# Optimization experiments

Measured on AMD Instinct MI355X. Metric: run time of the kernel, lower is better.

Reference implementation:

```python
import jax, jax.numpy as jnp
import numpy as np

N = 50000      # num nodes
E = 800000     # num edges (avg degree 16)
F_IN = 64      # num_node_features
H = 128        # hidden_channels (GatedGraphConv out_channels)
C = 16         # num_classes
L = 3          # num_layers


def setup_inputs() -> dict:
    key = jax.random.key(0)
    ks = jax.random.split(key, 9)
    s = 0.05
    x = jax.random.normal(ks[0], (N, F_IN), dtype=jnp.float32)
    edge_index = jax.random.randint(ks[1], (2, E), 0, N, dtype=jnp.int64)
    # GatedGraphConv per-layer message weights [L, H, H]
    W = jax.random.normal(ks[2], (L, H, H), dtype=jnp.float32) * s
    # GRUCell params (torch layout: rows ordered [r, z, n])
    w_ih = jax.random.normal(ks[3], (3 * H, H), dtype=jnp.float32) * s
    w_hh = jax.random.normal(ks[4], (3 * H, H), dtype=jnp.float32) * s
    b_ih = jax.random.normal(ks[5], (3 * H,), dtype=jnp.float32) * s
    b_hh = jax.random.normal(ks[6], (3 * H,), dtype=jnp.float32) * s
    # final classifier
    lin_w = jax.random.normal(ks[7], (C, H), dtype=jnp.float32) * s
    lin_b = jax.random.normal(ks[8], (C,), dtype=jnp.float32) * s
    return {"x": x, "edge_index": edge_index, "W": W, "w_ih": w_ih,
            "w_hh": w_hh, "b_ih": b_ih, "b_hh": b_hh,
            "lin_w": lin_w, "lin_b": lin_b}


def _gru_cell(m, h, w_ih, w_hh, b_ih, b_hh):
    # torch.nn.GRUCell: gates ordered r, z, n
    gi = m @ w_ih.T + b_ih   # [N, 3H]
    gh = h @ w_hh.T + b_hh   # [N, 3H]
    ir, iz, in_ = jnp.split(gi, 3, axis=1)
    hr, hz, hn = jnp.split(gh, 3, axis=1)
    r = jax.nn.sigmoid(ir + hr)
    z = jax.nn.sigmoid(iz + hz)
    n = jnp.tanh(in_ + r * hn)
    return (1.0 - z) * n + z * h


def reference(x, edge_index, W, w_ih, w_hh, b_ih, b_hh, lin_w, lin_b):
    # GatedGraphConv: zero-pad x to out_channels
    h = jnp.pad(x, ((0, 0), (0, H - F_IN)))  # [N, H]
    src = edge_index[0]  # message source (x_j)
    dst = edge_index[1]  # aggregation target
    for i in range(L):  # small fixed layer count
        m = h @ W[i]                                      # [N, H]
        agg = jax.ops.segment_sum(m[src], dst, num_segments=N)  # scatter-add
        h = _gru_cell(agg, h, w_ih, w_hh, b_ih, b_hh)
    out = h @ lin_w.T + lin_b                             # [N, C]
    return jax.nn.log_softmax(out, axis=1)
```

## Files before the change

### kernel.cpp

```cpp
#include <hip/hip_runtime.h>
#include <hip/hip_bf16.h>
#include <math.h>

#define H 128

typedef __bf16 bf16x8 __attribute__((ext_vector_type(8)));
typedef float f32x4 __attribute__((ext_vector_type(4)));
typedef __hip_bfloat16 bf16;

__device__ __forceinline__ bf16x8 ldb8(const bf16* p) {
  return *(const bf16x8*)(const void*)p;
}
__device__ __forceinline__ bf16x8 ldb8o(const bf16* base, unsigned byteoff) {
  return *(const bf16x8*)(const void*)((const char*)base + byteoff);
}
__device__ __forceinline__ float fsig(float x) {
  return __fdividef(1.f, 1.f + __expf(-x));
}
__device__ __forceinline__ float ftanh(float x) {
  float x2 = fminf(fmaxf(2.f * x, -80.f), 80.f);
  float t = __expf(x2);
  return __fdividef(t - 1.f, t + 1.f);
}

__global__ __launch_bounds__(256) void k_prep(const float* __restrict__ x,
                                              bf16* __restrict__ hb,
                                              const float* __restrict__ whh,
                                              bf16* __restrict__ whhb,
                                              const float* __restrict__ W,
                                              const float* __restrict__ wih,
                                              bf16* __restrict__ G,
                                              const int* __restrict__ dst,
                                              int* __restrict__ deg,
                                              int N, int E) {
  int i = blockIdx.x * 256 + threadIdx.x;
  int NH_ = N * H;
  if (i < NH_) {
    int f = i & (H - 1);
    int n = i >> 7;
    hb[i] = __float2bfloat16((f < 64) ? x[n * 64 + f] : 0.f);
    return;
  }
  i -= NH_;
  if (i < 3 * H * H) {
    whhb[i] = __float2bfloat16(whh[i]);
    return;
  }
  i -= 3 * H * H;
  if (i < 3 * 3 * H * H) {
    int l = i / (3 * H * H);
    int r = i % (3 * H * H);
    int j = r >> 7;
    int k = r & (H - 1);
    const float4* a = (const float4*)(wih + (size_t)j * H);
    const float4* b = (const float4*)(W + (size_t)l * H * H + (size_t)k * H);
    float s = 0.f;
#pragma unroll
    for (int q = 0; q < 32; q++) {
      float4 av = a[q], bv = b[q];
      s += av.x * bv.x + av.y * bv.y + av.z * bv.z + av.w * bv.w;
    }
    G[i] = __float2bfloat16(s);
    return;
  }
  i -= 3 * 3 * H * H;
  if (i < E) atomicAdd(&deg[dst[i]], 1);
}

__global__ __launch_bounds__(256) void k_bsum(const int* __restrict__ deg,
                                              int* __restrict__ bsums, int N) {
  __shared__ int ws[4];
  int t = threadIdx.x;
  int i = blockIdx.x * 256 + t;
  int v = (i < N) ? deg[i] : 0;
#pragma unroll
  for (int d = 1; d < 64; d <<= 1) v += __shfl_xor(v, d, 64);
  if ((t & 63) == 0) ws[t >> 6] = v;
  __syncthreads();
  if (t == 0) bsums[blockIdx.x] = ws[0] + ws[1] + ws[2] + ws[3];
}

__global__ __launch_bounds__(256) void k_bscan(int* __restrict__ bsums, int nb) {
  __shared__ int ws[4];
  int t = threadIdx.x;
  int lane = t & 63, w = t >> 6;
  int v = (t < nb) ? bsums[t] : 0;
  int s = v;
#pragma unroll
  for (int d = 1; d < 64; d <<= 1) {
    int u = __shfl_up(s, d, 64);
    if (lane >= d) s += u;
  }
  if (lane == 63) ws[w] = s;
  __syncthreads();
  int woff = 0;
  if (w >= 1) woff += ws[0];
  if (w >= 2) woff += ws[1];
  if (w >= 3) woff += ws[2];
  if (t < nb) bsums[t] = woff + s - v;
}

__global__ __launch_bounds__(256) void k_scan2(const int* __restrict__ deg,
                                               const int* __restrict__ bsums,
                                               int* __restrict__ rowptr,
                                               int* __restrict__ cursor,
                                               int N, int E) {
  __shared__ int ws[4];
  int t = threadIdx.x;
  int lane = t & 63, w = t >> 6;
  int i = blockIdx.x * 256 + t;
  int v = (i < N) ? deg[i] : 0;
  int s = v;
#pragma unroll
  for (int d = 1; d < 64; d <<= 1) {
    int u = __shfl_up(s, d, 64);
    if (lane >= d) s += u;
  }
  if (lane == 63) ws[w] = s;
  __syncthreads();
  int woff = 0;
  if (w >= 1) woff += ws[0];
  if (w >= 2) woff += ws[1];
  if (w >= 3) woff += ws[2];
  int excl = bsums[blockIdx.x] + woff + s - v;
  if (i < N) { rowptr[i] = excl; cursor[i] = excl; }
  if (i == 0) rowptr[N] = E;
}

__global__ __launch_bounds__(256) void k_fill(const int* __restrict__ src,
                                              const int* __restrict__ dst,
                                              int* __restrict__ cursor,
                                              int* __restrict__ csr_src, int E) {
  int e = blockIdx.x * 256 + threadIdx.x;
  if (e < E) {
    int pos = atomicAdd(&cursor[dst[e]], 1);
    csr_src[pos] = src[e];
  }
}

#define ASTRIDE 136
#define FSTRIDE 132
__global__ __launch_bounds__(512) void k_layer(const bf16* __restrict__ hbin,
                                               bf16* __restrict__ hbout,
                                               const bf16* __restrict__ Gl,
                                               const bf16* __restrict__ whhb,
                                               const float* __restrict__ bih,
                                               const float* __restrict__ bhh,
                                               const int* __restrict__ rowptr,
                                               const int* __restrict__ csr_src,
                                               const float* __restrict__ lw,
                                               const float* __restrict__ lb,
                                               float* __restrict__ out,
                                               int N) {
  __shared__ bf16 SH[64 * ASTRIDE];
  bf16* As = SH;
  bf16* Hs = SH + 32 * ASTRIDE;
  int t = threadIdx.x;
  int lane = t & 63;
  int wu = __builtin_amdgcn_readfirstlane(t >> 6);
  int row0 = blockIdx.x * 32;

  {
    int rl = t >> 4;
    int cc = t & 15;
    int row = row0 + rl; if (row > N - 1) row = N - 1;
    *(bf16x8*)(&Hs[rl * ASTRIDE + cc * 8]) = ldb8(hbin + (size_t)row * H + cc * 8);
  }

  int base = row0 + wu * 4;
  int rp[5];
#pragma unroll
  for (int j = 0; j < 5; j++) {
    int rw = base + j; if (rw > N) rw = N;
    rp[j] = rowptr[rw];
  }

  int e4 = lane >> 4;
  int c = lane & 15;
  unsigned coff = (unsigned)c << 4;

  int idxr[4];
#pragma unroll
  for (int rr = 0; rr < 4; rr++) {
    int rb = rp[rr];
    int n = rp[rr + 1] - rb; if (n > 64) n = 64;
    idxr[rr] = (lane < n) ? csr_src[rb + lane] : 0;
  }

  float acc[4][8];
#pragma unroll
  for (int rr = 0; rr < 4; rr++)
#pragma unroll
    for (int j = 0; j < 8; j++) acc[rr][j] = 0.f;

#pragma unroll
  for (int rr = 0; rr < 4; rr++) {
    int n = rp[rr + 1] - rp[rr];
    bf16x8 vv[8];
    float sc[8];
#pragma unroll
    for (int k = 0; k < 8; k++) {
      int s = e4 + 4 * k;
      int on = s < n;
      int ie = __shfl(idxr[rr], on ? s : 0, 64);
      vv[k] = ldb8o(hbin, ((unsigned)ie << 8) | coff);
      sc[k] = on ? 1.f : 0.f;
    }
#pragma unroll
    for (int k = 0; k < 8; k++) {
#pragma unroll
      for (int j = 0; j < 8; j++)
        acc[rr][j] = fmaf(sc[k], (float)vv[k][j], acc[rr][j]);
    }
    if (n > 32) {
      int hi = (n < 64) ? n : 64;
      for (int s0 = 32; s0 < hi; s0 += 4) {
        int s = s0 + e4;
        int on = s < hi;
        int ie = __shfl(idxr[rr], on ? s : 0, 64);
        bf16x8 v = ldb8o(hbin, ((unsigned)ie << 8) | coff);
        float scl = on ? 1.f : 0.f;
#pragma unroll
        for (int j = 0; j < 8; j++) acc[rr][j] = fmaf(scl, (float)v[j], acc[rr][j]);
      }
      int rb = rp[rr], re = rp[rr + 1];
      for (int b0 = rb + 64; b0 < re; b0 += 64) {
        int n2 = re - b0; if (n2 > 64) n2 = 64;
        int idx2 = (lane < n2) ? csr_src[b0 + lane] : 0;
        for (int s0 = 0; s0 < n2; s0 += 4) {
          int s = s0 + e4;
          int on = s < n2;
          int ie = __shfl(idx2, on ? s : 0, 64);
          bf16x8 v = ldb8o(hbin, ((unsigned)ie << 8) | coff);
          float scl = on ? 1.f : 0.f;
#pragma unroll
          for (int j = 0; j < 8; j++) acc[rr][j] = fmaf(scl, (float)v[j], acc[rr][j]);
        }
      }
    }
  }

#pragma unroll
  for (int rr = 0; rr < 4; rr++) {
#pragma unroll
    for (int j = 0; j < 8; j++) {
      acc[rr][j] += __shfl_xor(acc[rr][j], 16, 64);
      acc[rr][j] += __shfl_xor(acc[rr][j], 32, 64);
    }
    if (e4 == 0) {
      int rl = wu * 4 + rr;
      bf16x8 o;
#pragma unroll
      for (int j = 0; j < 8; j++) o[j] = (__bf16)acc[rr][j];
      *(bf16x8*)(&As[rl * ASTRIDE + c * 8]) = o;
    }
  }
  __syncthreads();

  int r = lane & 15, quad = lane >> 4, laneK = quad * 8;
  unsigned col = (unsigned)(wu * 16 + r);
  unsigned wg0 = col << 8;
  unsigned wg1 = (1u << 15) | wg0;
  unsigned wg2 = (2u << 15) | wg0;

  f32x4 aIR[2], aIZ[2], aIN[2], aHR[2], aHZ[2], aHN[2];
#pragma unroll
  for (int q = 0; q < 2; q++) {
    aIR[q] = (f32x4){0.f, 0.f, 0.f, 0.f};
    aIZ[q] = aIR[q]; aIN[q] = aIR[q];
    aHR[q] = aIR[q]; aHZ[q] = aIR[q]; aHN[q] = aIR[q];
  }

#pragma unroll
  for (int kb = 0; kb < 4; kb++) {
    int ko = kb * 32 + laneK;
    unsigned ko2 = (unsigned)(ko << 1);
    bf16x8 a0 = *(const bf16x8*)(&As[r * ASTRIDE + ko]);
    bf16x8 a1 = *(const bf16x8*)(&As[(16 + r) * ASTRIDE + ko]);
    bf16x8 h0 = *(const bf16x8*)(&Hs[r * ASTRIDE + ko]);
    bf16x8 h1 = *(const bf16x8*)(&Hs[(16 + r) * ASTRIDE + ko]);
    bf16x8 gr = ldb8o(Gl, wg0 | ko2);
    aIR[0] = __builtin_amdgcn_mfma_f32_16x16x32_bf16(a0, gr, aIR[0], 0, 0, 0);
    aIR[1] = __builtin_amdgcn_mfma_f32_16x16x32_bf16(a1, gr, aIR[1], 0, 0, 0);
    bf16x8 gz = ldb8o(Gl, wg1 | ko2);
    aIZ[0] = __builtin_amdgcn_mfma_f32_16x16x32_bf16(a0, gz, aIZ[0], 0, 0, 0);
    aIZ[1] = __builtin_amdgcn_mfma_f32_16x16x32_bf16(a1, gz, aIZ[1], 0, 0, 0);
    bf16x8 gn = ldb8o(Gl, wg2 | ko2);
    aIN[0] = __builtin_amdgcn_mfma_f32_16x16x32_bf16(a0, gn, aIN[0], 0, 0, 0);
    aIN[1] = __builtin_amdgcn_mfma_f32_16x16x32_bf16(a1, gn, aIN[1], 0, 0, 0);
    bf16x8 ur = ldb8o(whhb, wg0 | ko2);
    aHR[0] = __builtin_amdgcn_mfma_f32_16x16x32_bf16(h0, ur, aHR[0], 0, 0, 0);
    aHR[1] = __builtin_amdgcn_mfma_f32_16x16x32_bf16(h1, ur, aHR[1], 0, 0, 0);
    bf16x8 uz = ldb8o(whhb, wg1 | ko2);
    aHZ[0] = __builtin_amdgcn_mfma_f32_16x16x32_bf16(h0, uz, aHZ[0], 0, 0, 0);
    aHZ[1] = __builtin_amdgcn_mfma_f32_16x16x32_bf16(h1, uz, aHZ[1], 0, 0, 0);
    bf16x8 un = ldb8o(whhb, wg2 | ko2);
    aHN[0] = __builtin_amdgcn_mfma_f32_16x16x32_bf16(h0, un, aHN[0], 0, 0, 0);
    aHN[1] = __builtin_amdgcn_mfma_f32_16x16x32_bf16(h1, un, aHN[1], 0, 0, 0);
  }

  float bir = bih[col], biz = bih[H + col], bin = bih[2 * H + col];
  float bhr = bhh[col], bhz = bhh[H + col], bhn = bhh[2 * H + col];
  float hpv[2][4];
#pragma unroll
  for (int q = 0; q < 2; q++) {
#pragma unroll
    for (int i = 0; i < 4; i++) {
      int lrow = q * 16 + quad * 4 + i;
      float rg = fsig(aIR[q][i] + bir + aHR[q][i] + bhr);
      float zg = fsig(aIZ[q][i] + biz + aHZ[q][i] + bhz);
      float ng = ftanh(aIN[q][i] + bin + rg * (aHN[q][i] + bhn));
      float hold = __bfloat162float(Hs[lrow * ASTRIDE + col]);
      hpv[q][i] = (1.f - zg) * ng + zg * hold;
    }
  }
  __syncthreads();

  bf16* Sb = SH;
  float* Sf = (float*)SH;
#pragma unroll
  for (int q = 0; q < 2; q++) {
#pragma unroll
    for (int i = 0; i < 4; i++) {
      int lrow = q * 16 + quad * 4 + i;
      if (out) Sf[lrow * FSTRIDE + col] = hpv[q][i];
      else Sb[lrow * ASTRIDE + col] = __float2bfloat16(hpv[q][i]);
    }
  }
  __syncthreads();

  if (!out) {
    int rl = t >> 4;
    int cc = t & 15;
    int row = row0 + rl;
    if (row < N) {
      bf16x8 v = *(const bf16x8*)(&Sb[rl * ASTRIDE + cc * 8]);
      *(bf16x8*)(hbout + (size_t)row * H + cc * 8) = v;
    }
  } else {
    int cc = lane & 15;
    int q2 = lane >> 4;
    f32x4 wv[8];
    const float* wrow = lw + (size_t)cc * H + q2 * 32;
#pragma unroll
    for (int k = 0; k < 8; k++) wv[k] = *(const f32x4*)(wrow + k * 4);
    float bias = lb[cc];
#pragma unroll
    for (int rr = 0; rr < 4; rr++) {
      int lrow = wu * 4 + rr;
      int row = row0 + lrow;
      if (row >= N) continue;
      const float* hrow = &Sf[lrow * FSTRIDE + q2 * 32];
      float p = 0.f;
#pragma unroll
      for (int k = 0; k < 8; k++) {
        f32x4 hv = *(const f32x4*)(hrow + k * 4);
        p += hv[0] * wv[k][0] + hv[1] * wv[k][1] + hv[2] * wv[k][2] + hv[3] * wv[k][3];
      }
      p += __shfl_xor(p, 16, 64);
      p += __shfl_xor(p, 32, 64);
      float z = p + bias;
      float mx = z;
#pragma unroll
      for (int d = 1; d < 16; d <<= 1) mx = fmaxf(mx, __shfl_xor(mx, d, 64));
      float e = expf(z - mx);
      float ssum = e;
#pragma unroll
      for (int d = 1; d < 16; d <<= 1) ssum += __shfl_xor(ssum, d, 64);
      if (q2 == 0) out[(size_t)row * 16 + cc] = z - mx - logf(ssum);
    }
  }
}

extern "C" void kernel_launch(void* const* d_in, const int* in_sizes, int n_in,
                              void* d_out, int out_size, void* d_ws, size_t ws_size,
                              hipStream_t stream) {
  const float* x   = (const float*)d_in[0];
  const int*   ei  = (const int*)d_in[1];
  const float* W   = (const float*)d_in[2];
  const float* wih = (const float*)d_in[3];
  const float* whh = (const float*)d_in[4];
  const float* bih = (const float*)d_in[5];
  const float* bhh = (const float*)d_in[6];
  const float* lw  = (const float*)d_in[7];
  const float* lb  = (const float*)d_in[8];
  float* out = (float*)d_out;

  int N = in_sizes[0] / 64;
  int E = in_sizes[1] / 2;
  const int* src = ei;
  const int* dst = ei + E;

  size_t NH = (size_t)N * H;
  bf16* hb0  = (bf16*)d_ws;
  bf16* hb1  = hb0 + NH;
  bf16* Gb   = hb1 + NH;
  bf16* whhb = Gb + 3 * 3 * H * H;
  int* deg     = (int*)(whhb + 3 * H * H);
  int* rowptr  = deg + N;
  int* cursor  = rowptr + N + 1;
  int* bsums   = cursor + N;
  int* csr_src = bsums + 256;

  int nb_e = (E + 255) / 256;
  int nb_n = (N + 255) / 256;

  hipMemsetAsync(deg, 0, (size_t)N * sizeof(int), stream);
  int totalPrep = (int)NH + 3 * H * H + 3 * 3 * H * H + E;
  k_prep<<<(totalPrep + 255) / 256, 256, 0, stream>>>(x, hb0, whh, whhb, W, wih,
                                                      Gb, dst, deg, N, E);
  k_bsum<<<nb_n, 256, 0, stream>>>(deg, bsums, N);
  k_bscan<<<1, 256, 0, stream>>>(bsums, nb_n);
  k_scan2<<<nb_n, 256, 0, stream>>>(deg, bsums, rowptr, cursor, N, E);
  k_fill<<<nb_e, 256, 0, stream>>>(src, dst, cursor, csr_src, E);

  int nb_layer = (N + 31) / 32;
  bf16* hbp[2] = {hb0, hb1};
  for (int l = 0; l < 3; l++) {
    bf16* hin  = hbp[l & 1];
    bf16* hout = hbp[(l + 1) & 1];
    k_layer<<<nb_layer, 512, 0, stream>>>(hin, hout, Gb + (size_t)l * 3 * H * H,
                                          whhb, bih, bhh, rowptr, csr_src,
                                          lw, lb, (l == 2) ? out : nullptr, N);
  }
}
```

Before: 410.9 us.

## Halve rows per block to 16 and add short-degree gather fast path

The layer kernel now runs 256-thread blocks over 16 destination rows instead of 512-thread blocks over 32. Each wave computes 32 GRU output columns for a single 16-row MFMA tile, where before it computed 16 columns for two row tiles. This raises the occupancy hint and doubles the number of blocks, at the cost of loading each weight fragment once per 16 rows instead of once per 32. The neighbour gather gets a fast path for rows with at most 16 edges, issuing 4 slot loads instead of 8, which cuts wasted masked loads at the average degree of 16.

Measured after the change: 467.6 us. 13.8% more time.

```diff
diff --git a/kernel.cpp b/kernel.cpp
--- a/kernel.cpp
+++ b/kernel.cpp
@@ -21,6 +21,28 @@
   float x2 = fminf(fmaxf(2.f * x, -80.f), 80.f);
   float t = __expf(x2);
   return __fdividef(t - 1.f, t + 1.f);
+}
+
+template <int KB, int KE>
+__device__ __forceinline__ void gslots(const bf16* __restrict__ hbin, int idxw,
+                                       int n, int e4, unsigned coff,
+                                       float* __restrict__ acc) {
+  bf16x8 vv[KE - KB];
+  float sc[KE - KB];
+#pragma unroll
+  for (int k = KB; k < KE; k++) {
+    int s = e4 + 4 * k;
+    int on = s < n;
+    int ie = __shfl(idxw, on ? s : 0, 64);
+    vv[k - KB] = ldb8o(hbin, ((unsigned)ie << 8) | coff);
+    sc[k - KB] = on ? 1.f : 0.f;
+  }
+#pragma unroll
+  for (int k = 0; k < KE - KB; k++) {
+#pragma unroll
+    for (int j = 0; j < 8; j++)
+      acc[j] = fmaf(sc[k], (float)vv[k][j], acc[j]);
+  }
 }
 
 __global__ __launch_bounds__(256) void k_prep(const float* __restrict__ x,
@@ -140,7 +162,7 @@
 
 #define ASTRIDE 136
 #define FSTRIDE 132
-__global__ __launch_bounds__(512) void k_layer(const bf16* __restrict__ hbin,
+__global__ __launch_bounds__(256, 4) void k_layer(const bf16* __restrict__ hbin,
                                                bf16* __restrict__ hbout,
                                                const bf16* __restrict__ Gl,
                                                const bf16* __restrict__ whhb,
@@ -152,13 +174,13 @@
                                                const float* __restrict__ lb,
                                                float* __restrict__ out,
                                                int N) {
-  __shared__ bf16 SH[64 * ASTRIDE];
+  __shared__ bf16 SH[32 * ASTRIDE];
   bf16* As = SH;
-  bf16* Hs = SH + 32 * ASTRIDE;
+  bf16* Hs = SH + 16 * ASTRIDE;
   int t = threadIdx.x;
   int lane = t & 63;
   int wu = __builtin_amdgcn_readfirstlane(t >> 6);
-  int row0 = blockIdx.x * 32;
+  int row0 = blockIdx.x * 16;
 
   {
     int rl = t >> 4;
@@ -196,45 +218,34 @@
 #pragma unroll
   for (int rr = 0; rr < 4; rr++) {
     int n = rp[rr + 1] - rp[rr];
-    bf16x8 vv[8];
-    float sc[8];
-#pragma unroll
-    for (int k = 0; k < 8; k++) {
-      int s = e4 + 4 * k;
-      int on = s < n;
-      int ie = __shfl(idxr[rr], on ? s : 0, 64);
-      vv[k] = ldb8o(hbin, ((unsigned)ie << 8) | coff);
-      sc[k] = on ? 1.f : 0.f;
-    }
-#pragma unroll
-    for (int k = 0; k < 8; k++) {
-#pragma unroll
-      for (int j = 0; j < 8; j++)
-        acc[rr][j] = fmaf(sc[k], (float)vv[k][j], acc[rr][j]);
-    }
-    if (n > 32) {
-      int hi = (n < 64) ? n : 64;
-      for (int s0 = 32; s0 < hi; s0 += 4) {
-        int s = s0 + e4;
-        int on = s < hi;
-        int ie = __shfl(idxr[rr], on ? s : 0, 64);
-        bf16x8 v = ldb8o(hbin, ((unsigned)ie << 8) | coff);
-        float scl = on ? 1.f : 0.f;
-#pragma unroll
-        for (int j = 0; j < 8; j++) acc[rr][j] = fmaf(scl, (float)v[j], acc[rr][j]);
-      }
-      int rb = rp[rr], re = rp[rr + 1];
-      for (int b0 = rb + 64; b0 < re; b0 += 64) {
-        int n2 = re - b0; if (n2 > 64) n2 = 64;
-        int idx2 = (lane < n2) ? csr_src[b0 + lane] : 0;
-        for (int s0 = 0; s0 < n2; s0 += 4) {
+    if (n <= 16) {
+      gslots<0, 4>(hbin, idxr[rr], n, e4, coff, acc[rr]);
+    } else {
+      gslots<0, 8>(hbin, idxr[rr], n, e4, coff, acc[rr]);
+      if (n > 32) {
+        int hi = (n < 64) ? n : 64;
+        for (int s0 = 32; s0 < hi; s0 += 4) {
           int s = s0 + e4;
-          int on = s < n2;
-          int ie = __shfl(idx2, on ? s : 0, 64);
+          int on = s < hi;
+          int ie = __shfl(idxr[rr], on ? s : 0, 64);
           bf16x8 v = ldb8o(hbin, ((unsigned)ie << 8) | coff);
           float scl = on ? 1.f : 0.f;
 #pragma unroll
           for (int j = 0; j < 8; j++) acc[rr][j] = fmaf(scl, (float)v[j], acc[rr][j]);
+        }
+        int rb = rp[rr], re = rp[rr + 1];
+        for (int b0 = rb + 64; b0 < re; b0 += 64) {
+          int n2 = re - b0; if (n2 > 64) n2 = 64;
+          int idx2 = (lane < n2) ? csr_src[b0 + lane] : 0;
+          for (int s0 = 0; s0 < n2; s0 += 4) {
+            int s = s0 + e4;
+            int on = s < n2;
+            int ie = __shfl(idx2, on ? s : 0, 64);
+            bf16x8 v = ldb8o(hbin, ((unsigned)ie << 8) | coff);
+            float scl = on ? 1.f : 0.f;
+#pragma unroll
+            for (int j = 0; j < 8; j++) acc[rr][j] = fmaf(scl, (float)v[j], acc[rr][j]);
+          }
         }
       }
     }
@@ -258,17 +269,15 @@
   __syncthreads();
 
   int r = lane & 15, quad = lane >> 4, laneK = quad * 8;
-  unsigned col = (unsigned)(wu * 16 + r);
-  unsigned wg0 = col << 8;
-  unsigned wg1 = (1u << 15) | wg0;
-  unsigned wg2 = (2u << 15) | wg0;
+  unsigned col0 = (unsigned)(wu * 32 + r);
+  unsigned wgA[2] = {col0 << 8, (col0 + 16) << 8};
 
   f32x4 aIR[2], aIZ[2], aIN[2], aHR[2], aHZ[2], aHN[2];
 #pragma unroll
-  for (int q = 0; q < 2; q++) {
-    aIR[q] = (f32x4){0.f, 0.f, 0.f, 0.f};
-    aIZ[q] = aIR[q]; aIN[q] = aIR[q];
-    aHR[q] = aIR[q]; aHZ[q] = aIR[q]; aHN[q] = aIR[q];
+  for (int g = 0; g < 2; g++) {
+    aIR[g] = (f32x4){0.f, 0.f, 0.f, 0.f};
+    aIZ[g] = aIR[g]; aIN[g] = aIR[g];
+    aHR[g] = aIR[g]; aHZ[g] = aIR[g]; aHN[g] = aIR[g];
   }
 
 #pragma unroll
@@ -276,42 +285,39 @@
     int ko = kb * 32 + laneK;
     unsigned ko2 = (unsigned)(ko << 1);
     bf16x8 a0 = *(const bf16x8*)(&As[r * ASTRIDE + ko]);
-    bf16x8 a1 = *(const bf16x8*)(&As[(16 + r) * ASTRIDE + ko]);
     bf16x8 h0 = *(const bf16x8*)(&Hs[r * ASTRIDE + ko]);
-    bf16x8 h1 = *(const bf16x8*)(&Hs[(16 + r) * ASTRIDE + ko]);
-    bf16x8 gr = ldb8o(Gl, wg0 | ko2);
-    aIR[0] = __builtin_amdgcn_mfma_f32_16x16x32_bf16(a0, gr, aIR[0], 0, 0, 0);
-    aIR[1] = __builtin_amdgcn_mfma_f32_16x16x32_bf16(a1, gr, aIR[1], 0, 0, 0);
-    bf16x8 gz = ldb8o(Gl, wg1 | ko2);
-    aIZ[0] = __builtin_amdgcn_mfma_f32_16x16x32_bf16(a0, gz, aIZ[0], 0, 0, 0);
-    aIZ[1] = __builtin_amdgcn_mfma_f32_16x16x32_bf16(a1, gz, aIZ[1], 0, 0, 0);
-    bf16x8 gn = ldb8o(Gl, wg2 | ko2);
-    aIN[0] = __builtin_amdgcn_mfma_f32_16x16x32_bf16(a0, gn, aIN[0], 0, 0, 0);
-    aIN[1] = __builtin_amdgcn_mfma_f32_16x16x32_bf16(a1, gn, aIN[1], 0, 0, 0);
-    bf16x8 ur = ldb8o(whhb, wg0 | ko2);
-    aHR[0] = __builtin_amdgcn_mfma_f32_16x16x32_bf16(h0, ur, aHR[0], 0, 0, 0);
-    aHR[1] = __builtin_amdgcn_mfma_f32_16x16x32_bf16(h1, ur, aHR[1], 0, 0, 0);
-    bf16x8 uz = ldb8o(whhb, wg1 | ko2);
-    aHZ[0] = __builtin_amdgcn_mfma_f32_16x16x32_bf16(h0, uz, aHZ[0], 0, 0, 0);
-    aHZ[1] = __builtin_amdgcn_mfma_f32_16x16x32_bf16(h1, uz, aHZ[1], 0, 0, 0);
-    bf16x8 un = ldb8o(whhb, wg2 | ko2);
-    aHN[0] = __builtin_amdgcn_mfma_f32_16x16x32_bf16(h0, un, aHN[0], 0, 0, 0);
-    aHN[1] = __builtin_amdgcn_mfma_f32_16x16x32_bf16(h1, un, aHN[1], 0, 0, 0);
-  }
-
-  float bir = bih[col], biz = bih[H + col], bin = bih[2 * H + col];
-  float bhr = bhh[col], bhz = bhh[H + col], bhn = bhh[2 * H + col];
+#pragma unroll
+    for (int g = 0; g < 2; g++) {
+      unsigned w0 = wgA[g] | ko2;
+      bf16x8 gr = ldb8o(Gl, w0);
+      aIR[g] = __builtin_amdgcn_mfma_f32_16x16x32_bf16(a0, gr, aIR[g], 0, 0, 0);
+      bf16x8 gz = ldb8o(Gl, (1u << 15) | w0);
+      aIZ[g] = __builtin_amdgcn_mfma_f32_16x16x32_bf16(a0, gz, aIZ[g], 0, 0, 0);
+      bf16x8 gn = ldb8o(Gl, (2u << 15) | w0);
+      aIN[g] = __builtin_amdgcn_mfma_f32_16x16x32_bf16(a0, gn, aIN[g], 0, 0, 0);
+      bf16x8 ur = ldb8o(whhb, w0);
+      aHR[g] = __builtin_amdgcn_mfma_f32_16x16x32_bf16(h0, ur, aHR[g], 0, 0, 0);
+      bf16x8 uz = ldb8o(whhb, (1u << 15) | w0);
+      aHZ[g] = __builtin_amdgcn_mfma_f32_16x16x32_bf16(h0, uz, aHZ[g], 0, 0, 0);
+      bf16x8 un = ldb8o(whhb, (2u << 15) | w0);
+      aHN[g] = __builtin_amdgcn_mfma_f32_16x16x32_bf16(h0, un, aHN[g], 0, 0, 0);
+    }
+  }
+
   float hpv[2][4];
 #pragma unroll
-  for (int q = 0; q < 2; q++) {
+  for (int g = 0; g < 2; g++) {
+    int col = wu * 32 + g * 16 + r;
+    float bir = bih[col], biz = bih[H + col], bin = bih[2 * H + col];
+    float bhr = bhh[col], bhz = bhh[H + col], bhn = bhh[2 * H + col];
 #pragma unroll
     for (int i = 0; i < 4; i++) {
-      int lrow = q * 16 + quad * 4 + i;
-      float rg = fsig(aIR[q][i] + bir + aHR[q][i] + bhr);
-      float zg = fsig(aIZ[q][i] + biz + aHZ[q][i] + bhz);
-      float ng = ftanh(aIN[q][i] + bin + rg * (aHN[q][i] + bhn));
+      int lrow = quad * 4 + i;
+      float rg = fsig(aIR[g][i] + bir + aHR[g][i] + bhr);
+      float zg = fsig(aIZ[g][i] + biz + aHZ[g][i] + bhz);
+      float ng = ftanh(aIN[g][i] + bin + rg * (aHN[g][i] + bhn));
       float hold = __bfloat162float(Hs[lrow * ASTRIDE + col]);
-      hpv[q][i] = (1.f - zg) * ng + zg * hold;
+      hpv[g][i] = (1.f - zg) * ng + zg * hold;
     }
   }
   __syncthreads();
@@ -319,12 +325,13 @@
   bf16* Sb = SH;
   float* Sf = (float*)SH;
 #pragma unroll
-  for (int q = 0; q < 2; q++) {
+  for (int g = 0; g < 2; g++) {
+    int col = wu * 32 + g * 16 + r;
 #pragma unroll
     for (int i = 0; i < 4; i++) {
-      int lrow = q * 16 + quad * 4 + i;
-      if (out) Sf[lrow * FSTRIDE + col] = hpv[q][i];
-      else Sb[lrow * ASTRIDE + col] = __float2bfloat16(hpv[q][i]);
+      int lrow = quad * 4 + i;
+      if (out) Sf[lrow * FSTRIDE + col] = hpv[g][i];
+      else Sb[lrow * ASTRIDE + col] = __float2bfloat16(hpv[g][i]);
     }
   }
   __syncthreads();
@@ -414,12 +421,12 @@
   k_scan2<<<nb_n, 256, 0, stream>>>(deg, bsums, rowptr, cursor, N, E);
   k_fill<<<nb_e, 256, 0, stream>>>(src, dst, cursor, csr_src, E);
 
-  int nb_layer = (N + 31) / 32;
+  int nb_layer = (N + 15) / 16;
   bf16* hbp[2] = {hb0, hb1};
   for (int l = 0; l < 3; l++) {
     bf16* hin  = hbp[l & 1];
     bf16* hout = hbp[(l + 1) & 1];
-    k_layer<<<nb_layer, 512, 0, stream>>>(hin, hout, Gb + (size_t)l * 3 * H * H,
+    k_layer<<<nb_layer, 256, 0, stream>>>(hin, hout, Gb + (size_t)l * 3 * H * H,
                                           whhb, bih, bhh, rowptr, csr_src,
                                           lw, lb, (l == 2) ? out : nullptr, N);
   }
```

## Halve rows per layer block and fold block-sum into degree atomics

Applied to the files above, without the earlier changes.

The layer kernel now processes 16 rows per 512-thread block instead of 32. Each wave gathers 2 rows instead of 4, and the GRU MFMA step runs one 16-row tile. This doubles the block count, which is meant to give more parallelism and lower register pressure for the latency-bound neighbour gather. The cost is that the G and W_hh weight fragments are reloaded for every 16 rows instead of every 32. Separately, the k_bsum kernel is removed: per-256-node block sums are now accumulated with a second atomicAdd in the prep kernel, saving a launch but adding atomic contention on about 196 counters.

Result: slower. 928.2 us (+125.9%).

```diff
diff --git a/kernel.cpp b/kernel.cpp
--- a/kernel.cpp
+++ b/kernel.cpp
@@ -32,6 +32,7 @@
                                               bf16* __restrict__ G,
                                               const int* __restrict__ dst,
                                               int* __restrict__ deg,
+                                              int* __restrict__ bsums,
                                               int N, int E) {
   int i = blockIdx.x * 256 + threadIdx.x;
   int NH_ = N * H;
@@ -64,20 +65,11 @@
     return;
   }
   i -= 3 * 3 * H * H;
-  if (i < E) atomicAdd(&deg[dst[i]], 1);
-}
-
-__global__ __launch_bounds__(256) void k_bsum(const int* __restrict__ deg,
-                                              int* __restrict__ bsums, int N) {
-  __shared__ int ws[4];
-  int t = threadIdx.x;
-  int i = blockIdx.x * 256 + t;
-  int v = (i < N) ? deg[i] : 0;
-#pragma unroll
-  for (int d = 1; d < 64; d <<= 1) v += __shfl_xor(v, d, 64);
-  if ((t & 63) == 0) ws[t >> 6] = v;
-  __syncthreads();
-  if (t == 0) bsums[blockIdx.x] = ws[0] + ws[1] + ws[2] + ws[3];
+  if (i < E) {
+    int d = dst[i];
+    atomicAdd(&deg[d], 1);
+    atomicAdd(&bsums[d >> 8], 1);
+  }
 }
 
 __global__ __launch_bounds__(256) void k_bscan(int* __restrict__ bsums, int nb) {
@@ -152,25 +144,25 @@
                                                const float* __restrict__ lb,
                                                float* __restrict__ out,
                                                int N) {
-  __shared__ bf16 SH[64 * ASTRIDE];
+  __shared__ bf16 SH[32 * ASTRIDE];
   bf16* As = SH;
-  bf16* Hs = SH + 32 * ASTRIDE;
+  bf16* Hs = SH + 16 * ASTRIDE;
   int t = threadIdx.x;
   int lane = t & 63;
   int wu = __builtin_amdgcn_readfirstlane(t >> 6);
-  int row0 = blockIdx.x * 32;
-
-  {
+  int row0 = blockIdx.x * 16;
+
+  if (t < 256) {
     int rl = t >> 4;
     int cc = t & 15;
     int row = row0 + rl; if (row > N - 1) row = N - 1;
     *(bf16x8*)(&Hs[rl * ASTRIDE + cc * 8]) = ldb8(hbin + (size_t)row * H + cc * 8);
   }
 
-  int base = row0 + wu * 4;
-  int rp[5];
-#pragma unroll
-  for (int j = 0; j < 5; j++) {
+  int base = row0 + wu * 2;
+  int rp[3];
+#pragma unroll
+  for (int j = 0; j < 3; j++) {
     int rw = base + j; if (rw > N) rw = N;
     rp[j] = rowptr[rw];
   }
@@ -179,22 +171,22 @@
   int c = lane & 15;
   unsigned coff = (unsigned)c << 4;
 
-  int idxr[4];
-#pragma unroll
-  for (int rr = 0; rr < 4; rr++) {
+  int idxr[2];
+#pragma unroll
+  for (int rr = 0; rr < 2; rr++) {
     int rb = rp[rr];
     int n = rp[rr + 1] - rb; if (n > 64) n = 64;
     idxr[rr] = (lane < n) ? csr_src[rb + lane] : 0;
   }
 
-  float acc[4][8];
-#pragma unroll
-  for (int rr = 0; rr < 4; rr++)
+  float acc[2][8];
+#pragma unroll
+  for (int rr = 0; rr < 2; rr++)
 #pragma unroll
     for (int j = 0; j < 8; j++) acc[rr][j] = 0.f;
 
 #pragma unroll
-  for (int rr = 0; rr < 4; rr++) {
+  for (int rr = 0; rr < 2; rr++) {
     int n = rp[rr + 1] - rp[rr];
     bf16x8 vv[8];
     float sc[8];
@@ -241,14 +233,14 @@
   }
 
 #pragma unroll
-  for (int rr = 0; rr < 4; rr++) {
+  for (int rr = 0; rr < 2; rr++) {
 #pragma unroll
     for (int j = 0; j < 8; j++) {
       acc[rr][j] += __shfl_xor(acc[rr][j], 16, 64);
       acc[rr][j] += __shfl_xor(acc[rr][j], 32, 64);
     }
     if (e4 == 0) {
-      int rl = wu * 4 + rr;
+      int rl = wu * 2 + rr;
       bf16x8 o;
 #pragma unroll
       for (int j = 0; j < 8; j++) o[j] = (__bf16)acc[rr][j];
@@ -263,79 +255,62 @@
   unsigned wg1 = (1u << 15) | wg0;
   unsigned wg2 = (2u << 15) | wg0;
 
-  f32x4 aIR[2], aIZ[2], aIN[2], aHR[2], aHZ[2], aHN[2];
-#pragma unroll
-  for (int q = 0; q < 2; q++) {
-    aIR[q] = (f32x4){0.f, 0.f, 0.f, 0.f};
-    aIZ[q] = aIR[q]; aIN[q] = aIR[q];
-    aHR[q] = aIR[q]; aHZ[q] = aIR[q]; aHN[q] = aIR[q];
-  }
+  f32x4 aIR = (f32x4){0.f, 0.f, 0.f, 0.f};
+  f32x4 aIZ = aIR, aIN = aIR, aHR = aIR, aHZ = aIR, aHN = aIR;
 
 #pragma unroll
   for (int kb = 0; kb < 4; kb++) {
     int ko = kb * 32 + laneK;
     unsigned ko2 = (unsigned)(ko << 1);
     bf16x8 a0 = *(const bf16x8*)(&As[r * ASTRIDE + ko]);
-    bf16x8 a1 = *(const bf16x8*)(&As[(16 + r) * ASTRIDE + ko]);
     bf16x8 h0 = *(const bf16x8*)(&Hs[r * ASTRIDE + ko]);
-    bf16x8 h1 = *(const bf16x8*)(&Hs[(16 + r) * ASTRIDE + ko]);
     bf16x8 gr = ldb8o(Gl, wg0 | ko2);
-    aIR[0] = __builtin_amdgcn_mfma_f32_16x16x32_bf16(a0, gr, aIR[0], 0, 0, 0);
-    aIR[1] = __builtin_amdgcn_mfma_f32_16x16x32_bf16(a1, gr, aIR[1], 0, 0, 0);
+    aIR = __builtin_amdgcn_mfma_f32_16x16x32_bf16(a0, gr, aIR, 0, 0, 0);
     bf16x8 gz = ldb8o(Gl, wg1 | ko2);
-    aIZ[0] = __builtin_amdgcn_mfma_f32_16x16x32_bf16(a0, gz, aIZ[0], 0, 0, 0);
-    aIZ[1] = __builtin_amdgcn_mfma_f32_16x16x32_bf16(a1, gz, aIZ[1], 0, 0, 0);
+    aIZ = __builtin_amdgcn_mfma_f32_16x16x32_bf16(a0, gz, aIZ, 0, 0, 0);
     bf16x8 gn = ldb8o(Gl, wg2 | ko2);
-    aIN[0] = __builtin_amdgcn_mfma_f32_16x16x32_bf16(a0, gn, aIN[0], 0, 0, 0);
-    aIN[1] = __builtin_amdgcn_mfma_f32_16x16x32_bf16(a1, gn, aIN[1], 0, 0, 0);
+    aIN = __builtin_amdgcn_mfma_f32_16x16x32_bf16(a0, gn, aIN, 0, 0, 0);
     bf16x8 ur = ldb8o(whhb, wg0 | ko2);
-    aHR[0] = __builtin_amdgcn_mfma_f32_16x16x32_bf16(h0, ur, aHR[0], 0, 0, 0);
-    aHR[1] = __builtin_amdgcn_mfma_f32_16x16x32_bf16(h1, ur, aHR[1], 0, 0, 0);
+    aHR = __builtin_amdgcn_mfma_f32_16x16x32_bf16(h0, ur, aHR, 0, 0, 0);
     bf16x8 uz = ldb8o(whhb, wg1 | ko2);
-    aHZ[0] = __builtin_amdgcn_mfma_f32_16x16x32_bf16(h0, uz, aHZ[0], 0, 0, 0);
-    aHZ[1] = __builtin_amdgcn_mfma_f32_16x16x32_bf16(h1, uz, aHZ[1], 0, 0, 0);
+    aHZ = __builtin_amdgcn_mfma_f32_16x16x32_bf16(h0, uz, aHZ, 0, 0, 0);
     bf16x8 un = ldb8o(whhb, wg2 | ko2);
-    aHN[0] = __builtin_amdgcn_mfma_f32_16x16x32_bf16(h0, un, aHN[0], 0, 0, 0);
-    aHN[1] = __builtin_amdgcn_mfma_f32_16x16x32_bf16(h1, un, aHN[1], 0, 0, 0);
+    aHN = __builtin_amdgcn_mfma_f32_16x16x32_bf16(h0, un, aHN, 0, 0, 0);
   }
 
   float bir = bih[col], biz = bih[H + col], bin = bih[2 * H + col];
   float bhr = bhh[col], bhz = bhh[H + col], bhn = bhh[2 * H + col];
-  float hpv[2][4];
-#pragma unroll
-  for (int q = 0; q < 2; q++) {
-#pragma unroll
-    for (int i = 0; i < 4; i++) {
-      int lrow = q * 16 + quad * 4 + i;
-      float rg = fsig(aIR[q][i] + bir + aHR[q][i] + bhr);
-      float zg = fsig(aIZ[q][i] + biz + aHZ[q][i] + bhz);
-      float ng = ftanh(aIN[q][i] + bin + rg * (aHN[q][i] + bhn));
-      float hold = __bfloat162float(Hs[lrow * ASTRIDE + col]);
-      hpv[q][i] = (1.f - zg) * ng + zg * hold;
-    }
+  float hpv[4];
+#pragma unroll
+  for (int i = 0; i < 4; i++) {
+    int lrow = quad * 4 + i;
+    float rg = fsig(aIR[i] + bir + aHR[i] + bhr);
+    float zg = fsig(aIZ[i] + biz + aHZ[i] + bhz);
+    float ng = ftanh(aIN[i] + bin + rg * (aHN[i] + bhn));
+    float hold = __bfloat162float(Hs[lrow * ASTRIDE + col]);
+    hpv[i] = (1.f - zg) * ng + zg * hold;
   }
   __syncthreads();
 
   bf16* Sb = SH;
   float* Sf = (float*)SH;
 #pragma unroll
-  for (int q = 0; q < 2; q++) {
-#pragma unroll
-    for (int i = 0; i < 4; i++) {
-      int lrow = q * 16 + quad * 4 + i;
-      if (out) Sf[lrow * FSTRIDE + col] = hpv[q][i];
-      else Sb[lrow * ASTRIDE + col] = __float2bfloat16(hpv[q][i]);
-    }
+  for (int i = 0; i < 4; i++) {
+    int lrow = quad * 4 + i;
+    if (out) Sf[lrow * FSTRIDE + col] = hpv[i];
+    else Sb[lrow * ASTRIDE + col] = __float2bfloat16(hpv[i]);
   }
   __syncthreads();
 
   if (!out) {
-    int rl = t >> 4;
-    int cc = t & 15;
-    int row = row0 + rl;
-    if (row < N) {
-      bf16x8 v = *(const bf16x8*)(&Sb[rl * ASTRIDE + cc * 8]);
-      *(bf16x8*)(hbout + (size_t)row * H + cc * 8) = v;
+    if (t < 256) {
+      int rl = t >> 4;
+      int cc = t & 15;
+      int row = row0 + rl;
+      if (row < N) {
+        bf16x8 v = *(const bf16x8*)(&Sb[rl * ASTRIDE + cc * 8]);
+        *(bf16x8*)(hbout + (size_t)row * H + cc * 8) = v;
+      }
     }
   } else {
     int cc = lane & 15;
@@ -346,8 +321,8 @@
     for (int k = 0; k < 8; k++) wv[k] = *(const f32x4*)(wrow + k * 4);
     float bias = lb[cc];
 #pragma unroll
-    for (int rr = 0; rr < 4; rr++) {
-      int lrow = wu * 4 + rr;
+    for (int rr = 0; rr < 2; rr++) {
+      int lrow = wu * 2 + rr;
       int row = row0 + lrow;
       if (row >= N) continue;
       const float* hrow = &Sf[lrow * FSTRIDE + q2 * 32];
@@ -397,24 +372,23 @@
   bf16* Gb   = hb1 + NH;
   bf16* whhb = Gb + 3 * 3 * H * H;
   int* deg     = (int*)(whhb + 3 * H * H);
-  int* rowptr  = deg + N;
+  int* bsums   = deg + N;
+  int* rowptr  = bsums + 256;
   int* cursor  = rowptr + N + 1;
-  int* bsums   = cursor + N;
-  int* csr_src = bsums + 256;
+  int* csr_src = cursor + N;
 
   int nb_e = (E + 255) / 256;
   int nb_n = (N + 255) / 256;
 
-  hipMemsetAsync(deg, 0, (size_t)N * sizeof(int), stream);
+  hipMemsetAsync(deg, 0, (size_t)(N + 256) * sizeof(int), stream);
   int totalPrep = (int)NH + 3 * H * H + 3 * 3 * H * H + E;
   k_prep<<<(totalPrep + 255) / 256, 256, 0, stream>>>(x, hb0, whh, whhb, W, wih,
-                                                      Gb, dst, deg, N, E);
-  k_bsum<<<nb_n, 256, 0, stream>>>(deg, bsums, N);
+                                                      Gb, dst, deg, bsums, N, E);
   k_bscan<<<1, 256, 0, stream>>>(bsums, nb_n);
   k_scan2<<<nb_n, 256, 0, stream>>>(deg, bsums, rowptr, cursor, N, E);
   k_fill<<<nb_e, 256, 0, stream>>>(src, dst, cursor, csr_src, E);
 
-  int nb_layer = (N + 31) / 32;
+  int nb_layer = (N + 15) / 16;
   bf16* hbp[2] = {hb0, hb1};
   for (int l = 0; l < 3; l++) {
     bf16* hin  = hbp[l & 1];
```
